# Optimization experiments

Hardware: AMD Instinct MI355X
Metric: run time of the kernel (lower is better)

The kernel has to match this reference:

```python
import jax, jax.numpy as jnp
import numpy as np

B, H, M, D, L, V, T = 32, 3, 2048, 512, 32, 32000, 2049


def _position_encoding(sent_len, dim):
    # standard MemN2N position encoding l_{jk} = (1 - j/J) - (k/d)(1 - 2j/J)
    j = np.arange(1, sent_len + 1, dtype=np.float32)[:, None]
    k = np.arange(1, dim + 1, dtype=np.float32)[None, :]
    enc = (1.0 - j / sent_len) - (k / dim) * (1.0 - 2.0 * j / sent_len)
    return jnp.asarray(enc, dtype=jnp.float32)


def setup_inputs() -> dict:
    key = jax.random.key(0)
    ks = jax.random.split(key, 8)
    return {
        "query": jax.random.randint(ks[0], (B, L), 0, V),
        "rel_time": jax.random.randint(ks[1], (B, M), 0, T),
        "key_mems": jax.random.normal(ks[2], (B, H, M, D), jnp.float32) * 0.1,
        "val_mems": jax.random.normal(ks[3], (B, H, M, D), jnp.float32) * 0.1,
        "B_emb": jax.random.normal(ks[4], (V, D), jnp.float32) * 0.1,
        "TA": jax.random.normal(ks[5], (H, T, D), jnp.float32) * 0.1,
        "TC": jax.random.normal(ks[6], (H, T, D), jnp.float32) * 0.1,
        "pos_enc": _position_encoding(L, D),
    }


def reference(query, rel_time, key_mems, val_mems, B_emb, TA, TC, pos_enc):
    # query embedding: [B, L, D] * [L, D] summed over sentence positions -> u [B, 1, D]
    u = (B_emb[query] * pos_enc[None, :, :]).sum(axis=1, keepdims=True)

    num_hops = TA.shape[0]
    for i in range(num_hops):  # small fixed hop count (3)
        key_time = TA[i][rel_time]            # [B, M, D]
        val_time = TC[i][rel_time]            # [B, M, D]
        key_mem = key_mems[:, i, :, :] + key_time
        val_mem = val_mems[:, i, :, :] + val_time
        logit = (key_mem * u).sum(axis=2)      # [B, M] additive (dot) score vs u
        p = jax.nn.softmax(logit, axis=1)      # [B, M]
        o = (val_mem * p[:, :, None]).sum(axis=1, keepdims=True)  # [B, 1, D]
        u = o + u                              # recurrent query update
    return u  # [B, 1, D] final controller state (fed to W in qa_forward)
```

## Files before the change

### kernel.cpp

```cpp
#include <hip/hip_runtime.h>

#define BB 32
#define HH 3
#define MM 2048
#define DD 512
#define LL 32
#define TT 2049
#define NCHUNK 32
#define MCHUNK (MM / NCHUNK)

__global__ __launch_bounds__(256) void qembed_kernel(
    const int* __restrict__ query, const float* __restrict__ B_emb,
    const float* __restrict__ pos_enc, float* __restrict__ u) {
    int b = blockIdx.x;
    int d0 = threadIdx.x * 2;
    float a0 = 0.f, a1 = 0.f;
#pragma unroll 4
    for (int l = 0; l < LL; ++l) {
        int q = query[b * LL + l];
        float2 e = *(const float2*)(B_emb + (size_t)q * DD + d0);
        float2 pe = *(const float2*)(pos_enc + l * DD + d0);
        a0 += e.x * pe.x;
        a1 += e.y * pe.y;
    }
    u[b * DD + d0] = a0;
    u[b * DD + d0 + 1] = a1;
}

__global__ __launch_bounds__(256) void fused_hop_kernel(
    const float* __restrict__ key_mems, const float* __restrict__ val_mems,
    const float* __restrict__ TA, const float* __restrict__ TC,
    const int* __restrict__ rel_time, const float* __restrict__ u,
    float* __restrict__ partials, float* __restrict__ pmx,
    float* __restrict__ ps, int hop) {
    __shared__ float sm[4][DD];
    __shared__ float smx[4];
    __shared__ float ssum[4];
    int b = blockIdx.y, c = blockIdx.x;
    int wave = threadIdx.x >> 6, lane = threadIdx.x & 63;
    int d0 = lane * 8;

    float4 u0 = *(const float4*)(u + b * DD + d0);
    float4 u1 = *(const float4*)(u + b * DD + d0 + 4);

    const size_t kbase = (size_t)(b * HH + hop) * MM * DD;

    float rmax = -3.4e38f, rsum = 0.f;
    float acc[8] = {0.f, 0.f, 0.f, 0.f, 0.f, 0.f, 0.f, 0.f};

#pragma unroll 2
    for (int j = 0; j < MCHUNK / 4; ++j) {
        int m = c * MCHUNK + j * 4 + wave;
        int t = rel_time[b * MM + m];
        const float* krow = key_mems + kbase + (size_t)m * DD + d0;
        const float* vrow = val_mems + kbase + (size_t)m * DD + d0;
        const float* arow = TA + (size_t)(hop * TT + t) * DD + d0;
        const float* crow = TC + (size_t)(hop * TT + t) * DD + d0;

        float4 k0 = *(const float4*)krow;
        float4 k1 = *(const float4*)(krow + 4);
        float4 a0 = *(const float4*)arow;
        float4 a1 = *(const float4*)(arow + 4);
        float4 v0 = *(const float4*)vrow;
        float4 v1 = *(const float4*)(vrow + 4);
        float4 c0 = *(const float4*)crow;
        float4 c1 = *(const float4*)(crow + 4);

        float dp = (k0.x + a0.x) * u0.x + (k0.y + a0.y) * u0.y +
                   (k0.z + a0.z) * u0.z + (k0.w + a0.w) * u0.w +
                   (k1.x + a1.x) * u1.x + (k1.y + a1.y) * u1.y +
                   (k1.z + a1.z) * u1.z + (k1.w + a1.w) * u1.w;
#pragma unroll
        for (int off = 32; off > 0; off >>= 1) dp += __shfl_xor(dp, off);

        float nm = fmaxf(rmax, dp);
        float scale = expf(rmax - nm);
        float w = expf(dp - nm);
        rsum = rsum * scale + w;
        acc[0] = acc[0] * scale + w * (v0.x + c0.x);
        acc[1] = acc[1] * scale + w * (v0.y + c0.y);
        acc[2] = acc[2] * scale + w * (v0.z + c0.z);
        acc[3] = acc[3] * scale + w * (v0.w + c0.w);
        acc[4] = acc[4] * scale + w * (v1.x + c1.x);
        acc[5] = acc[5] * scale + w * (v1.y + c1.y);
        acc[6] = acc[6] * scale + w * (v1.z + c1.z);
        acc[7] = acc[7] * scale + w * (v1.w + c1.w);
        rmax = nm;
    }

    if (lane == 0) {
        smx[wave] = rmax;
        ssum[wave] = rsum;
    }
    *(float4*)&sm[wave][d0] = make_float4(acc[0], acc[1], acc[2], acc[3]);
    *(float4*)&sm[wave][d0 + 4] = make_float4(acc[4], acc[5], acc[6], acc[7]);
    __syncthreads();

    float bmx = fmaxf(fmaxf(smx[0], smx[1]), fmaxf(smx[2], smx[3]));
    float e0 = expf(smx[0] - bmx);
    float e1 = expf(smx[1] - bmx);
    float e2 = expf(smx[2] - bmx);
    float e3 = expf(smx[3] - bmx);

    if (threadIdx.x == 0) {
        pmx[c * BB + b] = bmx;
        ps[c * BB + b] = ssum[0] * e0 + ssum[1] * e1 + ssum[2] * e2 + ssum[3] * e3;
    }
    int d = threadIdx.x * 2;
    float2 po;
    po.x = sm[0][d] * e0 + sm[1][d] * e1 + sm[2][d] * e2 + sm[3][d] * e3;
    po.y = sm[0][d + 1] * e0 + sm[1][d + 1] * e1 + sm[2][d + 1] * e2 +
           sm[3][d + 1] * e3;
    *(float2*)(partials + ((size_t)c * BB + b) * DD + d) = po;
}

__global__ __launch_bounds__(256) void combine_kernel(
    const float* __restrict__ partials, const float* __restrict__ pmx,
    const float* __restrict__ ps, float* __restrict__ u,
    float* __restrict__ out, int write_out) {
    __shared__ float sscale[NCHUNK];
    int b = blockIdx.x;
    int tid = threadIdx.x;

    float MX = -3.4e38f;
#pragma unroll
    for (int cc = 0; cc < NCHUNK; ++cc) MX = fmaxf(MX, pmx[cc * BB + b]);
    if (tid < NCHUNK) sscale[tid] = expf(pmx[tid * BB + b] - MX);
    __syncthreads();

    float S = 0.f;
#pragma unroll
    for (int cc = 0; cc < NCHUNK; ++cc) S += ps[cc * BB + b] * sscale[cc];
    float inv = 1.f / S;

    int d = tid * 2;
    float ox = 0.f, oy = 0.f;
#pragma unroll 4
    for (int cc = 0; cc < NCHUNK; ++cc) {
        float2 pv = *(const float2*)(partials + ((size_t)cc * BB + b) * DD + d);
        float sc = sscale[cc];
        ox += pv.x * sc;
        oy += pv.y * sc;
    }
    float2 uu = *(const float2*)(u + b * DD + d);
    uu.x += ox * inv;
    uu.y += oy * inv;
    *(float2*)(u + b * DD + d) = uu;
    if (write_out) *(float2*)(out + b * DD + d) = uu;
}

extern "C" void kernel_launch(void* const* d_in, const int* in_sizes, int n_in,
                              void* d_out, int out_size, void* d_ws, size_t ws_size,
                              hipStream_t stream) {
    const int* query = (const int*)d_in[0];
    const int* rel_time = (const int*)d_in[1];
    const float* key_mems = (const float*)d_in[2];
    const float* val_mems = (const float*)d_in[3];
    const float* B_emb = (const float*)d_in[4];
    const float* TA = (const float*)d_in[5];
    const float* TC = (const float*)d_in[6];
    const float* pos_enc = (const float*)d_in[7];
    float* out = (float*)d_out;

    float* ws = (float*)d_ws;
    float* u = ws;
    float* pmx = u + BB * DD;
    float* ps = pmx + NCHUNK * BB;
    float* partials = ps + NCHUNK * BB;

    qembed_kernel<<<BB, 256, 0, stream>>>(query, B_emb, pos_enc, u);

    for (int hop = 0; hop < HH; ++hop) {
        fused_hop_kernel<<<dim3(NCHUNK, BB), 256, 0, stream>>>(
            key_mems, val_mems, TA, TC, rel_time, u, partials, pmx, ps, hop);
        combine_kernel<<<BB, 256, 0, stream>>>(partials, pmx, ps, u, out,
                                               hop == HH - 1 ? 1 : 0);
    }
}
```

Baseline: 852.2 us.

## Split hop into logits, softmax with time-bin histogram, and value passes

Uses linearity to stop gathering TA/TC rows for every memory slot. TA·u is computed once per time index and added to key·u. The softmax weights are binned by rel_time so TC is read per distinct time index, not per memory slot. This removes two of the four per-slot row streams, which matters most in a memory-bound kernel. The cost is six launches per hop instead of two, plus extra round trips for the logits and bins through global memory. TA·u and the weighted TC sum are also now computed for every batch over all 2049 time rows.

```diff
diff --git a/kernel.cpp b/kernel.cpp
--- a/kernel.cpp
+++ b/kernel.cpp
@@ -8,6 +8,8 @@
 #define TT 2049
 #define NCHUNK 32
 #define MCHUNK (MM / NCHUNK)
+#define NT2 16
+#define TCH 129
 
 __global__ __launch_bounds__(256) void qembed_kernel(
     const int* __restrict__ query, const float* __restrict__ B_emb,
@@ -27,126 +29,181 @@
     u[b * DD + d0 + 1] = a1;
 }
 
-__global__ __launch_bounds__(256) void fused_hop_kernel(
-    const float* __restrict__ key_mems, const float* __restrict__ val_mems,
-    const float* __restrict__ TA, const float* __restrict__ TC,
-    const int* __restrict__ rel_time, const float* __restrict__ u,
-    float* __restrict__ partials, float* __restrict__ pmx,
-    float* __restrict__ ps, int hop) {
+__global__ __launch_bounds__(256) void tdot_kernel(
+    const float* __restrict__ TA, const float* __restrict__ u,
+    float* __restrict__ ta_dot, int hop) {
+    int b = blockIdx.y;
+    int wave = threadIdx.x >> 6, lane = threadIdx.x & 63;
+    int t = blockIdx.x * 4 + wave;
+    if (t >= TT) return;
+    int d0 = lane * 8;
+    const float* arow = TA + (size_t)(hop * TT + t) * DD + d0;
+    const float* urow = u + b * DD + d0;
+    float4 a0 = *(const float4*)arow;
+    float4 a1 = *(const float4*)(arow + 4);
+    float4 u0 = *(const float4*)urow;
+    float4 u1 = *(const float4*)(urow + 4);
+    float acc = a0.x * u0.x + a0.y * u0.y + a0.z * u0.z + a0.w * u0.w +
+                a1.x * u1.x + a1.y * u1.y + a1.z * u1.z + a1.w * u1.w;
+#pragma unroll
+    for (int off = 32; off > 0; off >>= 1) acc += __shfl_xor(acc, off);
+    if (lane == 0) ta_dot[b * TT + t] = acc;
+}
+
+__global__ __launch_bounds__(256) void logits_kernel(
+    const float* __restrict__ key_mems, const int* __restrict__ rel_time,
+    const float* __restrict__ u, const float* __restrict__ ta_dot,
+    float* __restrict__ logits, int hop) {
+    int b = blockIdx.y;
+    int wave = threadIdx.x >> 6, lane = threadIdx.x & 63;
+    int d0 = lane * 8;
+    float4 u0 = *(const float4*)(u + b * DD + d0);
+    float4 u1 = *(const float4*)(u + b * DD + d0 + 4);
+    const size_t kbase = (size_t)(b * HH + hop) * MM * DD;
+#pragma unroll
+    for (int j = 0; j < 4; ++j) {
+        int m = blockIdx.x * 16 + wave * 4 + j;
+        const float* krow = key_mems + kbase + (size_t)m * DD + d0;
+        float4 k0 = *(const float4*)krow;
+        float4 k1 = *(const float4*)(krow + 4);
+        float acc = k0.x * u0.x + k0.y * u0.y + k0.z * u0.z + k0.w * u0.w +
+                    k1.x * u1.x + k1.y * u1.y + k1.z * u1.z + k1.w * u1.w;
+#pragma unroll
+        for (int off = 32; off > 0; off >>= 1) acc += __shfl_xor(acc, off);
+        if (lane == 0)
+            logits[b * MM + m] = acc + ta_dot[b * TT + rel_time[b * MM + m]];
+    }
+}
+
+__global__ __launch_bounds__(256) void softmax_bins_kernel(
+    float* __restrict__ logits, const int* __restrict__ rel_time,
+    float* __restrict__ wbin) {
+    __shared__ float bins[TT];
+    __shared__ float smx[4];
+    __shared__ float ssm[4];
+    int b = blockIdx.x;
+    int tid = threadIdx.x;
+    int wave = tid >> 6, lane = tid & 63;
+    float* row = logits + b * MM;
+
+    for (int i = tid; i < TT; i += 256) bins[i] = 0.f;
+
+    float vals[8];
+    float mx = -3.4e38f;
+#pragma unroll
+    for (int j = 0; j < 8; ++j) {
+        vals[j] = row[j * 256 + tid];
+        mx = fmaxf(mx, vals[j]);
+    }
+#pragma unroll
+    for (int off = 32; off > 0; off >>= 1) mx = fmaxf(mx, __shfl_xor(mx, off));
+    if (lane == 0) smx[wave] = mx;
+    __syncthreads();
+    mx = fmaxf(fmaxf(smx[0], smx[1]), fmaxf(smx[2], smx[3]));
+
+    float s = 0.f;
+#pragma unroll
+    for (int j = 0; j < 8; ++j) {
+        vals[j] = expf(vals[j] - mx);
+        s += vals[j];
+    }
+#pragma unroll
+    for (int off = 32; off > 0; off >>= 1) s += __shfl_xor(s, off);
+    if (lane == 0) ssm[wave] = s;
+    __syncthreads();
+    s = (ssm[0] + ssm[1]) + (ssm[2] + ssm[3]);
+    float inv = 1.f / s;
+#pragma unroll
+    for (int j = 0; j < 8; ++j) {
+        float pv = vals[j] * inv;
+        row[j * 256 + tid] = pv;
+        int t = rel_time[b * MM + j * 256 + tid];
+        atomicAdd(&bins[t], pv);
+    }
+    __syncthreads();
+    for (int i = tid; i < TT; i += 256) wbin[b * TT + i] = bins[i];
+}
+
+__global__ __launch_bounds__(256) void weighted_kernel(
+    const float* __restrict__ val_mems, const float* __restrict__ p,
+    float* __restrict__ partials, int hop) {
     __shared__ float sm[4][DD];
-    __shared__ float smx[4];
-    __shared__ float ssum[4];
     int b = blockIdx.y, c = blockIdx.x;
     int wave = threadIdx.x >> 6, lane = threadIdx.x & 63;
     int d0 = lane * 8;
-
-    float4 u0 = *(const float4*)(u + b * DD + d0);
-    float4 u1 = *(const float4*)(u + b * DD + d0 + 4);
-
-    const size_t kbase = (size_t)(b * HH + hop) * MM * DD;
-
-    float rmax = -3.4e38f, rsum = 0.f;
+    const size_t vbase = (size_t)(b * HH + hop) * MM * DD;
+
     float acc[8] = {0.f, 0.f, 0.f, 0.f, 0.f, 0.f, 0.f, 0.f};
-
 #pragma unroll 2
     for (int j = 0; j < MCHUNK / 4; ++j) {
         int m = c * MCHUNK + j * 4 + wave;
-        int t = rel_time[b * MM + m];
-        const float* krow = key_mems + kbase + (size_t)m * DD + d0;
-        const float* vrow = val_mems + kbase + (size_t)m * DD + d0;
-        const float* arow = TA + (size_t)(hop * TT + t) * DD + d0;
-        const float* crow = TC + (size_t)(hop * TT + t) * DD + d0;
-
-        float4 k0 = *(const float4*)krow;
-        float4 k1 = *(const float4*)(krow + 4);
-        float4 a0 = *(const float4*)arow;
-        float4 a1 = *(const float4*)(arow + 4);
+        float pw = p[b * MM + m];
+        const float* vrow = val_mems + vbase + (size_t)m * DD + d0;
         float4 v0 = *(const float4*)vrow;
         float4 v1 = *(const float4*)(vrow + 4);
-        float4 c0 = *(const float4*)crow;
-        float4 c1 = *(const float4*)(crow + 4);
-
-        float dp = (k0.x + a0.x) * u0.x + (k0.y + a0.y) * u0.y +
-                   (k0.z + a0.z) * u0.z + (k0.w + a0.w) * u0.w +
-                   (k1.x + a1.x) * u1.x + (k1.y + a1.y) * u1.y +
-                   (k1.z + a1.z) * u1.z + (k1.w + a1.w) * u1.w;
-#pragma unroll
-        for (int off = 32; off > 0; off >>= 1) dp += __shfl_xor(dp, off);
-
-        float nm = fmaxf(rmax, dp);
-        float scale = expf(rmax - nm);
-        float w = expf(dp - nm);
-        rsum = rsum * scale + w;
-        acc[0] = acc[0] * scale + w * (v0.x + c0.x);
-        acc[1] = acc[1] * scale + w * (v0.y + c0.y);
-        acc[2] = acc[2] * scale + w * (v0.z + c0.z);
-        acc[3] = acc[3] * scale + w * (v0.w + c0.w);
-        acc[4] = acc[4] * scale + w * (v1.x + c1.x);
-        acc[5] = acc[5] * scale + w * (v1.y + c1.y);
-        acc[6] = acc[6] * scale + w * (v1.z + c1.z);
-        acc[7] = acc[7] * scale + w * (v1.w + c1.w);
-        rmax = nm;
-    }
-
-    if (lane == 0) {
-        smx[wave] = rmax;
-        ssum[wave] = rsum;
-    }
-    *(float4*)&sm[wave][d0] = make_float4(acc[0], acc[1], acc[2], acc[3]);
-    *(float4*)&sm[wave][d0 + 4] = make_float4(acc[4], acc[5], acc[6], acc[7]);
-    __syncthreads();
-
-    float bmx = fmaxf(fmaxf(smx[0], smx[1]), fmaxf(smx[2], smx[3]));
-    float e0 = expf(smx[0] - bmx);
-    float e1 = expf(smx[1] - bmx);
-    float e2 = expf(smx[2] - bmx);
-    float e3 = expf(smx[3] - bmx);
-
-    if (threadIdx.x == 0) {
-        pmx[c * BB + b] = bmx;
-        ps[c * BB + b] = ssum[0] * e0 + ssum[1] * e1 + ssum[2] * e2 + ssum[3] * e3;
-    }
-    int d = threadIdx.x * 2;
-    float2 po;
-    po.x = sm[0][d] * e0 + sm[1][d] * e1 + sm[2][d] * e2 + sm[3][d] * e3;
-    po.y = sm[0][d + 1] * e0 + sm[1][d + 1] * e1 + sm[2][d + 1] * e2 +
-           sm[3][d + 1] * e3;
-    *(float2*)(partials + ((size_t)c * BB + b) * DD + d) = po;
-}
-
-__global__ __launch_bounds__(256) void combine_kernel(
-    const float* __restrict__ partials, const float* __restrict__ pmx,
-    const float* __restrict__ ps, float* __restrict__ u,
-    float* __restrict__ out, int write_out) {
-    __shared__ float sscale[NCHUNK];
-    int b = blockIdx.x;
+        acc[0] += v0.x * pw;
+        acc[1] += v0.y * pw;
+        acc[2] += v0.z * pw;
+        acc[3] += v0.w * pw;
+        acc[4] += v1.x * pw;
+        acc[5] += v1.y * pw;
+        acc[6] += v1.z * pw;
+        acc[7] += v1.w * pw;
+    }
+#pragma unroll
+    for (int k = 0; k < 8; ++k) sm[wave][d0 + k] = acc[k];
+    __syncthreads();
+#pragma unroll
+    for (int r = 0; r < 2; ++r) {
+        int d = threadIdx.x * 2 + r;
+        float v = (sm[0][d] + sm[1][d]) + (sm[2][d] + sm[3][d]);
+        partials[((size_t)c * BB + b) * DD + d] = v;
+    }
+}
+
+__global__ __launch_bounds__(256) void tc_kernel(
+    const float* __restrict__ TC, const float* __restrict__ wbin,
+    float* __restrict__ partials2, int hop) {
+    __shared__ float wl[TCH];
+    int b = blockIdx.y, tc = blockIdx.x;
+    int t0 = tc * TCH;
     int tid = threadIdx.x;
-
-    float MX = -3.4e38f;
-#pragma unroll
-    for (int cc = 0; cc < NCHUNK; ++cc) MX = fmaxf(MX, pmx[cc * BB + b]);
-    if (tid < NCHUNK) sscale[tid] = expf(pmx[tid * BB + b] - MX);
-    __syncthreads();
-
-    float S = 0.f;
-#pragma unroll
-    for (int cc = 0; cc < NCHUNK; ++cc) S += ps[cc * BB + b] * sscale[cc];
-    float inv = 1.f / S;
-
+    for (int i = tid; i < TCH; i += 256) {
+        int t = t0 + i;
+        wl[i] = (t < TT) ? wbin[b * TT + t] : 0.f;
+    }
+    __syncthreads();
     int d = tid * 2;
-    float ox = 0.f, oy = 0.f;
-#pragma unroll 4
-    for (int cc = 0; cc < NCHUNK; ++cc) {
-        float2 pv = *(const float2*)(partials + ((size_t)cc * BB + b) * DD + d);
-        float sc = sscale[cc];
-        ox += pv.x * sc;
-        oy += pv.y * sc;
-    }
-    float2 uu = *(const float2*)(u + b * DD + d);
-    uu.x += ox * inv;
-    uu.y += oy * inv;
-    *(float2*)(u + b * DD + d) = uu;
-    if (write_out) *(float2*)(out + b * DD + d) = uu;
+    float ax = 0.f, ay = 0.f;
+    for (int i = 0; i < TCH; ++i) {
+        int t = t0 + i;
+        if (t >= TT) break;
+        float wv = wl[i];
+        if (wv != 0.f) {
+            float2 tcv = *(const float2*)(TC + (size_t)(hop * TT + t) * DD + d);
+            ax += wv * tcv.x;
+            ay += wv * tcv.y;
+        }
+    }
+    float2 o;
+    o.x = ax;
+    o.y = ay;
+    *(float2*)(partials2 + ((size_t)tc * BB + b) * DD + d) = o;
+}
+
+__global__ __launch_bounds__(256) void update_kernel(
+    const float* __restrict__ partials, const float* __restrict__ partials2,
+    float* __restrict__ u, float* __restrict__ out, int write_out) {
+    int idx = blockIdx.x * 256 + threadIdx.x;
+    float s = 0.f;
+#pragma unroll
+    for (int c = 0; c < NCHUNK; ++c) s += partials[(size_t)c * BB * DD + idx];
+#pragma unroll
+    for (int tc = 0; tc < NT2; ++tc)
+        s += partials2[(size_t)tc * BB * DD + idx];
+    float uu = u[idx] + s;
+    u[idx] = uu;
+    if (write_out) out[idx] = uu;
 }
 
 extern "C" void kernel_launch(void* const* d_in, const int* in_sizes, int n_in,
@@ -164,16 +221,24 @@
 
     float* ws = (float*)d_ws;
     float* u = ws;
-    float* pmx = u + BB * DD;
-    float* ps = pmx + NCHUNK * BB;
-    float* partials = ps + NCHUNK * BB;
+    float* logits = u + BB * DD;
+    float* ta_dot = logits + BB * MM;
+    float* wbin = ta_dot + BB * TT;
+    float* partials = wbin + BB * TT;
+    float* partials2 = partials + NCHUNK * BB * DD;
 
     qembed_kernel<<<BB, 256, 0, stream>>>(query, B_emb, pos_enc, u);
 
     for (int hop = 0; hop < HH; ++hop) {
-        fused_hop_kernel<<<dim3(NCHUNK, BB), 256, 0, stream>>>(
-            key_mems, val_mems, TA, TC, rel_time, u, partials, pmx, ps, hop);
-        combine_kernel<<<BB, 256, 0, stream>>>(partials, pmx, ps, u, out,
-                                               hop == HH - 1 ? 1 : 0);
-    }
-}
+        tdot_kernel<<<dim3((TT + 3) / 4, BB), 256, 0, stream>>>(
+            TA, u, ta_dot, hop);
+        logits_kernel<<<dim3(MM / 16, BB), 256, 0, stream>>>(
+            key_mems, rel_time, u, ta_dot, logits, hop);
+        softmax_bins_kernel<<<BB, 256, 0, stream>>>(logits, rel_time, wbin);
+        weighted_kernel<<<dim3(NCHUNK, BB), 256, 0, stream>>>(
+            val_mems, logits, partials, hop);
+        tc_kernel<<<dim3(NT2, BB), 256, 0, stream>>>(TC, wbin, partials2, hop);
+        update_kernel<<<BB * DD / 256, 256, 0, stream>>>(
+            partials, partials2, u, out, hop == HH - 1 ? 1 : 0);
+    }
+}
```

New measurement: 949.6 us. 11.4% more time.
